# Kernel optimization log

Measured on AMD Instinct MI355X. Metric: run time of the kernel, lower is better.

The kernel has to match this reference:

```python
import jax, jax.numpy as jnp
import numpy as np

B, L, D, H = 2, 2048, 1024, 16
HD = D // H  # head dim = 64


def setup_inputs() -> dict:
    key = jax.random.key(0)
    ks = jax.random.split(key, 6)
    s = 0.02
    return {
        "hidden_states": jax.random.normal(ks[0], (B, L, D), jnp.float32),
        "attention_mask": jnp.zeros((B, 1, 1, L), jnp.float32),
        "Wq": jax.random.normal(ks[1], (D, D), jnp.float32) * s,
        "bq": jnp.zeros((D,), jnp.float32),
        "Wk": jax.random.normal(ks[2], (D, D), jnp.float32) * s,
        "bk": jnp.zeros((D,), jnp.float32),
        "Wv": jax.random.normal(ks[3], (D, D), jnp.float32) * s,
        "bv": jnp.zeros((D,), jnp.float32),
        "Wo": jax.random.normal(ks[4], (D, D), jnp.float32) * s,
        "bo": jnp.zeros((D,), jnp.float32),
    }


def reference(hidden_states, attention_mask, Wq, bq, Wk, bk, Wv, bv, Wo, bo):
    # Linear projections (torch Linear: x @ W.T + b; here W stored as [in,out])
    q = hidden_states @ Wq + bq  # [B,L,D]
    k = hidden_states @ Wk + bk
    v = hidden_states @ Wv + bv

    def split_heads(x):  # [B,L,D] -> [B,H,L,HD]
        return x.reshape(B, L, H, HD).transpose(0, 2, 1, 3)

    q, k, v = split_heads(q), split_heads(k), split_heads(v)

    scores = jnp.einsum("bhqd,bhkd->bhqk", q, k) / jnp.sqrt(
        jnp.asarray(HD, q.dtype)
    )
    scores = scores + attention_mask  # additive mask, broadcast [B,1,1,L]
    pdtype = scores.dtype
    # fp32 upcast around softmax, as in the original module
    probs = jax.nn.softmax(scores.astype(jnp.float32), axis=-1).astype(pdtype)
    # dropout prob = 0 (eval) -> identity; head_mask=None
    ctx = jnp.einsum("bhqk,bhkd->bhqd", probs, v)  # [B,H,L,HD]
    ctx = ctx.transpose(0, 2, 1, 3).reshape(B, L, D)
    out = ctx @ Wo + bo  # BertSelfOutput_preLN dense (dropout=0)
    return out
```

## Files before the change

### kernel.cpp

```cpp
#include <hip/hip_runtime.h>

#define BB 2
#define LL 2048
#define DDIM 1024
#define HH 16
#define HDIM 64
#define MM (BB*LL)
#define KK 1024
#define LOG2E 1.44269504f

typedef __attribute__((ext_vector_type(8))) short s8v;
typedef __attribute__((ext_vector_type(8))) unsigned short u8v;
typedef __attribute__((ext_vector_type(4))) float f4v;
typedef __attribute__((ext_vector_type(16))) float f16v;

__device__ __forceinline__ unsigned short f2bf(float f) {
    unsigned int u = __float_as_uint(f);
    u += 0x7fffu + ((u >> 16) & 1u);
    return (unsigned short)(u >> 16);
}

__device__ __forceinline__ float fexp2(float x) { return __builtin_amdgcn_exp2f(x); }

__device__ __forceinline__ void gld_lds16(const unsigned short* g, unsigned short* l) {
    __builtin_amdgcn_global_load_lds(
        (const __attribute__((address_space(1))) unsigned int*)g,
        (__attribute__((address_space(3))) unsigned int*)l, 16, 0, 0);
}

__global__ __launch_bounds__(256) void prep(
        const float* __restrict__ X,
        const float* __restrict__ Wq, const float* __restrict__ Wk,
        const float* __restrict__ Wv, const float* __restrict__ Wo,
        unsigned short* __restrict__ Xb,
        unsigned short* __restrict__ WqT, unsigned short* __restrict__ WkT,
        unsigned short* __restrict__ WvT, unsigned short* __restrict__ WoT) {
    __shared__ float lds[64][65];
    const int blk = blockIdx.x, t = threadIdx.x;
    if (blk < 4096) {
        int i = blk * 256 + t;
        float4 v = ((const float4*)X)[i];
        ushort4 r;
        r.x = f2bf(v.x); r.y = f2bf(v.y); r.z = f2bf(v.z); r.w = f2bf(v.w);
        ((ushort4*)Xb)[i] = r;
        return;
    }
    const int tb = blk - 4096;
    const int w = tb >> 8;
    const int tile = tb & 255;
    const int k0 = (tile >> 4) * 64, n0 = (tile & 15) * 64;
    const float* src; unsigned short* dst;
    switch (w) {
        case 0: src = Wq; dst = WqT; break;
        case 1: src = Wk; dst = WkT; break;
        case 2: src = Wv; dst = WvT; break;
        default: src = Wo; dst = WoT; break;
    }
    #pragma unroll
    for (int j = 0; j < 4; ++j) {
        int r = (t >> 4) + 16*j, c = (t & 15) * 4;
        float4 v = *(const float4*)(src + (size_t)(k0 + r) * DDIM + n0 + c);
        lds[r][c] = v.x; lds[r][c+1] = v.y; lds[r][c+2] = v.z; lds[r][c+3] = v.w;
    }
    __syncthreads();
    #pragma unroll
    for (int j = 0; j < 2; ++j) {
        int rr = (t >> 3) + 32*j, cc = (t & 7) * 8;
        u8v o;
        #pragma unroll
        for (int i = 0; i < 8; ++i) o[i] = f2bf(lds[cc + i][rr]);
        *(u8v*)(dst + (size_t)(n0 + rr) * KK + k0 + cc) = o;
    }
}

__device__ __forceinline__ void gemm_core(const unsigned short* __restrict__ A,
                                          const unsigned short* __restrict__ BT,
                                          int Mbase, int Nbase,
                                          unsigned short* As, unsigned short* Bs,
                                          f4v acc[4][4]) {
    const int t = threadIdx.x;
    const int lane = t & 63, wave = t >> 6;
    const int wm = wave & 1, wn = wave >> 1;
    const int l15 = lane & 15, quad = lane >> 4;
    const int srow = t >> 2, schunk = (t & 3) * 8;

    #pragma unroll
    for (int mt = 0; mt < 4; ++mt)
        #pragma unroll
        for (int nt = 0; nt < 4; ++nt)
            acc[mt][nt] = f4v{0.f, 0.f, 0.f, 0.f};

    const unsigned short* gA0 = A  + (size_t)(Mbase + srow)      * KK + schunk;
    const unsigned short* gA1 = A  + (size_t)(Mbase + 64 + srow) * KK + schunk;
    const unsigned short* gB0 = BT + (size_t)(Nbase + srow)      * KK + schunk;
    const unsigned short* gB1 = BT + (size_t)(Nbase + 64 + srow) * KK + schunk;

    for (int kb = 0; kb < KK; kb += 64) {
        __syncthreads();
        gld_lds16(gA0 + kb,      As + t*8);
        gld_lds16(gA1 + kb,      As + 2048 + t*8);
        gld_lds16(gA0 + kb + 32, As + 4096 + t*8);
        gld_lds16(gA1 + kb + 32, As + 4096 + 2048 + t*8);
        gld_lds16(gB0 + kb,      Bs + t*8);
        gld_lds16(gB1 + kb,      Bs + 2048 + t*8);
        gld_lds16(gB0 + kb + 32, Bs + 4096 + t*8);
        gld_lds16(gB1 + kb + 32, Bs + 4096 + 2048 + t*8);
        __syncthreads();
        #pragma unroll
        for (int kk = 0; kk < 2; ++kk) {
            const unsigned short* Ab = As + kk*4096;
            const unsigned short* Bb = Bs + kk*4096;
            s8v af[4], bfv[4];
            #pragma unroll
            for (int mt = 0; mt < 4; ++mt)
                af[mt] = *(const s8v*)(Ab + (wm*64 + mt*16 + l15)*32 + quad*8);
            #pragma unroll
            for (int nt = 0; nt < 4; ++nt)
                bfv[nt] = *(const s8v*)(Bb + (wn*64 + nt*16 + l15)*32 + quad*8);
            #pragma unroll
            for (int mt = 0; mt < 4; ++mt)
                #pragma unroll
                for (int nt = 0; nt < 4; ++nt)
                    acc[mt][nt] = __builtin_amdgcn_mfma_f32_16x16x32_bf16(af[mt], bfv[nt], acc[mt][nt], 0, 0, 0);
        }
    }
}

__global__ __launch_bounds__(256) void qkv_gemm(
        const unsigned short* __restrict__ Xb,
        const unsigned short* __restrict__ WqT, const unsigned short* __restrict__ WkT,
        const unsigned short* __restrict__ WvT,
        const float* __restrict__ bq, const float* __restrict__ bk, const float* __restrict__ bv,
        unsigned short* __restrict__ Qh, unsigned short* __restrict__ Kh,
        unsigned short* __restrict__ Vt) {
    __shared__ alignas(16) unsigned short As[128*64];
    __shared__ alignas(16) unsigned short Bs[128*64];
    const int mode = blockIdx.z;
    const unsigned short* BT = (mode == 0) ? WqT : (mode == 1) ? WkT : WvT;
    const float* bias        = (mode == 0) ? bq  : (mode == 1) ? bk  : bv;
    unsigned short* out      = (mode == 0) ? Qh  : (mode == 1) ? Kh  : Vt;
    const int Mbase = blockIdx.y * 128, Nbase = blockIdx.x * 128;

    f4v acc[4][4];
    gemm_core(Xb, BT, Mbase, Nbase, As, Bs, acc);

    const int lane = threadIdx.x & 63, wave = threadIdx.x >> 6;
    const int wm = wave & 1, wn = wave >> 1, l15 = lane & 15, quad = lane >> 4;
    #pragma unroll
    for (int mt = 0; mt < 4; ++mt)
        #pragma unroll
        for (int nt = 0; nt < 4; ++nt)
            #pragma unroll
            for (int r = 0; r < 4; ++r) {
                int gm = Mbase + wm*64 + mt*16 + quad*4 + r;
                int gn = Nbase + wn*64 + nt*16 + l15;
                float v = acc[mt][nt][r] + bias[gn];
                int bb = gm >> 11, ll = gm & 2047;
                int hh = gn >> 6,  dd = gn & 63;
                if (mode == 2)
                    out[((size_t)(bb*HH + hh)*HDIM + dd)*LL + ll] = f2bf(v);
                else
                    out[((size_t)(bb*HH + hh)*LL + ll)*HDIM + dd] = f2bf(v);
            }
}

__global__ __launch_bounds__(256) void attn(
        const unsigned short* __restrict__ Qh, const unsigned short* __restrict__ Kh,
        const unsigned short* __restrict__ Vt, const float* __restrict__ mask,
        unsigned short* __restrict__ ctx) {
    __shared__ alignas(16) unsigned short Ks[64*72];
    __shared__ alignas(16) unsigned short Vs[64*72];
    __shared__ alignas(16) unsigned short P [4*32*72];

    const int t = threadIdx.x, lane = t & 63, wave = t >> 6;
    const int l31 = lane & 31, hgrp = lane >> 5;

    const int n = blockIdx.x;
    const int bh = (n & 7) * 4 + ((n >> 3) & 3);
    const int qblk = n >> 5;
    const int b = bh >> 4, hh = bh & 15;

    const unsigned short* Qb = Qh + (size_t)bh * LL * HDIM;
    const unsigned short* Kb = Kh + (size_t)bh * LL * HDIM;
    const unsigned short* Vb = Vt + (size_t)bh * HDIM * LL;
    const float* mb = mask + (size_t)b * LL;
    const int q0 = qblk * 128 + wave * 32;
    unsigned short* Pw = P + wave * 32 * 72;

    const int srow = t >> 2, scol = (t & 3) * 16;

    s8v qf[4];
    #pragma unroll
    for (int hf = 0; hf < 4; ++hf)
        qf[hf] = *(const s8v*)(Qb + (size_t)(q0 + l31)*HDIM + hf*16 + hgrp*8);

    f16v o[2];
    #pragma unroll
    for (int nc = 0; nc < 2; ++nc)
        #pragma unroll
        for (int r = 0; r < 16; ++r) o[nc][r] = 0.f;
    float rs[16];
    #pragma unroll
    for (int r = 0; r < 16; ++r) rs[r] = 0.f;

    const float C1 = 0.125f * LOG2E;

    for (int kt = 0; kt < LL; kt += 64) {
        float4 ka  = *(const float4*)(Kb + (size_t)(kt + srow)*HDIM + scol);
        float4 kb2 = *(const float4*)(Kb + (size_t)(kt + srow)*HDIM + scol + 8);
        float4 va  = *(const float4*)(Vb + (size_t)srow*LL + kt + scol);
        float4 vb2 = *(const float4*)(Vb + (size_t)srow*LL + kt + scol + 8);
        float mv0 = mb[kt + l31] * LOG2E;
        float mv1 = mb[kt + 32 + l31] * LOG2E;

        __syncthreads();
        *(float4*)(Ks + srow*72 + scol)     = ka;
        *(float4*)(Ks + srow*72 + scol + 8) = kb2;
        *(float4*)(Vs + srow*72 + scol)     = va;
        *(float4*)(Vs + srow*72 + scol + 8) = vb2;
        __syncthreads();

        f16v sac[2];
        #pragma unroll
        for (int kc = 0; kc < 2; ++kc) {
            #pragma unroll
            for (int r = 0; r < 16; ++r) sac[kc][r] = 0.f;
            #pragma unroll
            for (int hf = 0; hf < 4; ++hf) {
                s8v kf = *(const s8v*)(Ks + (kc*32 + l31)*72 + hf*16 + hgrp*8);
                sac[kc] = __builtin_amdgcn_mfma_f32_32x32x16_bf16(qf[hf], kf, sac[kc], 0, 0, 0);
            }
        }
        #pragma unroll
        for (int kc = 0; kc < 2; ++kc) {
            float mvv = kc ? mv1 : mv0;
            #pragma unroll
            for (int r = 0; r < 16; ++r) {
                float p = fexp2(sac[kc][r] * C1 + mvv);
                rs[r] += p;
                int row = (r & 3) + 8*(r >> 2) + 4*hgrp;
                Pw[row*72 + kc*32 + l31] = f2bf(p);
            }
        }
        #pragma unroll
        for (int kt16 = 0; kt16 < 4; ++kt16) {
            s8v pf = *(const s8v*)(Pw + l31*72 + kt16*16 + hgrp*8);
            #pragma unroll
            for (int nc = 0; nc < 2; ++nc) {
                s8v vf = *(const s8v*)(Vs + (nc*32 + l31)*72 + kt16*16 + hgrp*8);
                o[nc] = __builtin_amdgcn_mfma_f32_32x32x16_bf16(pf, vf, o[nc], 0, 0, 0);
            }
        }
    }

    #pragma unroll
    for (int r = 0; r < 16; ++r) {
        float s0 = rs[r];
        s0 += __shfl_xor(s0, 1);
        s0 += __shfl_xor(s0, 2);
        s0 += __shfl_xor(s0, 4);
        s0 += __shfl_xor(s0, 8);
        s0 += __shfl_xor(s0, 16);
        rs[r] = 1.0f / s0;
    }
    #pragma unroll
    for (int r = 0; r < 16; ++r) {
        int row = (r & 3) + 8*(r >> 2) + 4*hgrp;
        int q = q0 + row;
        size_t base = ((size_t)b*LL + q)*DDIM + hh*HDIM;
        #pragma unroll
        for (int nc = 0; nc < 2; ++nc)
            ctx[base + nc*32 + l31] = f2bf(o[nc][r] * rs[r]);
    }
}

__global__ __launch_bounds__(256) void out_gemm(
        const unsigned short* __restrict__ Cb, const unsigned short* __restrict__ WoT,
        const float* __restrict__ bo, float* __restrict__ out) {
    __shared__ alignas(16) unsigned short As[128*64];
    __shared__ alignas(16) unsigned short Bs[64*64];
    const int t = threadIdx.x;
    const int lane = t & 63, wave = t >> 6;
    const int wm = wave & 1, wn = wave >> 1;
    const int l15 = lane & 15, quad = lane >> 4;
    const int srow = t >> 2, schunk = (t & 3) * 8;
    const int Mbase = blockIdx.y * 128, Nbase = blockIdx.x * 64;

    f4v acc[4][2];
    #pragma unroll
    for (int mt = 0; mt < 4; ++mt)
        #pragma unroll
        for (int nt = 0; nt < 2; ++nt)
            acc[mt][nt] = f4v{0.f, 0.f, 0.f, 0.f};

    const unsigned short* gA0 = Cb  + (size_t)(Mbase + srow)      * KK + schunk;
    const unsigned short* gA1 = Cb  + (size_t)(Mbase + 64 + srow) * KK + schunk;
    const unsigned short* gB0 = WoT + (size_t)(Nbase + srow)      * KK + schunk;

    for (int kb = 0; kb < KK; kb += 64) {
        __syncthreads();
        gld_lds16(gA0 + kb,      As + t*8);
        gld_lds16(gA1 + kb,      As + 2048 + t*8);
        gld_lds16(gA0 + kb + 32, As + 4096 + t*8);
        gld_lds16(gA1 + kb + 32, As + 4096 + 2048 + t*8);
        gld_lds16(gB0 + kb,      Bs + t*8);
        gld_lds16(gB0 + kb + 32, Bs + 2048 + t*8);
        __syncthreads();
        #pragma unroll
        for (int kk = 0; kk < 2; ++kk) {
            const unsigned short* Ab = As + kk*4096;
            const unsigned short* Bb = Bs + kk*2048;
            s8v af[4], bfv[2];
            #pragma unroll
            for (int mt = 0; mt < 4; ++mt)
                af[mt] = *(const s8v*)(Ab + (wm*64 + mt*16 + l15)*32 + quad*8);
            #pragma unroll
            for (int nt = 0; nt < 2; ++nt)
                bfv[nt] = *(const s8v*)(Bb + (wn*32 + nt*16 + l15)*32 + quad*8);
            #pragma unroll
            for (int mt = 0; mt < 4; ++mt)
                #pragma unroll
                for (int nt = 0; nt < 2; ++nt)
                    acc[mt][nt] = __builtin_amdgcn_mfma_f32_16x16x32_bf16(af[mt], bfv[nt], acc[mt][nt], 0, 0, 0);
        }
    }

    #pragma unroll
    for (int mt = 0; mt < 4; ++mt)
        #pragma unroll
        for (int nt = 0; nt < 2; ++nt)
            #pragma unroll
            for (int r = 0; r < 4; ++r) {
                int gm = Mbase + wm*64 + mt*16 + quad*4 + r;
                int gn = Nbase + wn*32 + nt*16 + l15;
                out[(size_t)gm*DDIM + gn] = acc[mt][nt][r] + bo[gn];
            }
}

extern "C" void kernel_launch(void* const* d_in, const int* in_sizes, int n_in,
                              void* d_out, int out_size, void* d_ws, size_t ws_size,
                              hipStream_t stream) {
    const float* X    = (const float*)d_in[0];
    const float* mask = (const float*)d_in[1];
    const float* Wq   = (const float*)d_in[2];
    const float* bq   = (const float*)d_in[3];
    const float* Wk   = (const float*)d_in[4];
    const float* bk   = (const float*)d_in[5];
    const float* Wv   = (const float*)d_in[6];
    const float* bv   = (const float*)d_in[7];
    const float* Wo   = (const float*)d_in[8];
    const float* bo   = (const float*)d_in[9];
    float* out = (float*)d_out;

    char* ws = (char*)d_ws;
    unsigned short* Xb  = (unsigned short*)(ws);
    unsigned short* WqT = (unsigned short*)(ws + (8u  << 20));
    unsigned short* WkT = (unsigned short*)(ws + (10u << 20));
    unsigned short* WvT = (unsigned short*)(ws + (12u << 20));
    unsigned short* WoT = (unsigned short*)(ws + (14u << 20));
    unsigned short* Qh  = (unsigned short*)(ws + (16u << 20));
    unsigned short* Kh  = (unsigned short*)(ws + (24u << 20));
    unsigned short* Vt  = (unsigned short*)(ws + (32u << 20));
    unsigned short* Cb  = Xb;

    prep     <<<dim3(5120),    dim3(256), 0, stream>>>(X, Wq, Wk, Wv, Wo, Xb, WqT, WkT, WvT, WoT);
    qkv_gemm <<<dim3(8,32,3),  dim3(256), 0, stream>>>(Xb, WqT, WkT, WvT, bq, bk, bv, Qh, Kh, Vt);
    attn     <<<dim3(512),     dim3(256), 0, stream>>>(Qh, Kh, Vt, mask, Cb);
    out_gemm <<<dim3(16,32),   dim3(256), 0, stream>>>(Cb, WoT, bo, out);
}
```

Baseline: 226.0 us.

## Stage QKV epilogue through LDS for vector stores, halve GEMM K-step

The QKV GEMM epilogue now writes biased bf16 results into shared memory in two halves, then emits 16-byte vectorized global stores. For V this performs the head transpose in LDS instead of scattered 2-byte strided writes. Both GEMMs drop from a 64-wide to a 32-wide K step with smaller LDS tiles, which lowers LDS use and may raise occupancy but doubles the number of barriers. The attention P conversion to bf16 now truncates instead of rounding, which saves a few ALU ops at a small accuracy cost.

New measurement: 222.9 us. About the same (-1.4%).

```diff
diff --git a/kernel.cpp b/kernel.cpp
--- a/kernel.cpp
+++ b/kernel.cpp
@@ -94,35 +94,30 @@
     const unsigned short* gA1 = A  + (size_t)(Mbase + 64 + srow) * KK + schunk;
     const unsigned short* gB0 = BT + (size_t)(Nbase + srow)      * KK + schunk;
     const unsigned short* gB1 = BT + (size_t)(Nbase + 64 + srow) * KK + schunk;
-
-    for (int kb = 0; kb < KK; kb += 64) {
-        __syncthreads();
-        gld_lds16(gA0 + kb,      As + t*8);
-        gld_lds16(gA1 + kb,      As + 2048 + t*8);
-        gld_lds16(gA0 + kb + 32, As + 4096 + t*8);
-        gld_lds16(gA1 + kb + 32, As + 4096 + 2048 + t*8);
-        gld_lds16(gB0 + kb,      Bs + t*8);
-        gld_lds16(gB1 + kb,      Bs + 2048 + t*8);
-        gld_lds16(gB0 + kb + 32, Bs + 4096 + t*8);
-        gld_lds16(gB1 + kb + 32, Bs + 4096 + 2048 + t*8);
-        __syncthreads();
-        #pragma unroll
-        for (int kk = 0; kk < 2; ++kk) {
-            const unsigned short* Ab = As + kk*4096;
-            const unsigned short* Bb = Bs + kk*4096;
-            s8v af[4], bfv[4];
-            #pragma unroll
-            for (int mt = 0; mt < 4; ++mt)
-                af[mt] = *(const s8v*)(Ab + (wm*64 + mt*16 + l15)*32 + quad*8);
+    unsigned short* lA0 = As + t*8;
+    unsigned short* lA1 = As + 64*32 + t*8;
+    unsigned short* lB0 = Bs + t*8;
+    unsigned short* lB1 = Bs + 64*32 + t*8;
+
+    for (int kb = 0; kb < KK; kb += 32) {
+        __syncthreads();
+        gld_lds16(gA0 + kb, lA0);
+        gld_lds16(gA1 + kb, lA1);
+        gld_lds16(gB0 + kb, lB0);
+        gld_lds16(gB1 + kb, lB1);
+        __syncthreads();
+        s8v af[4], bfv[4];
+        #pragma unroll
+        for (int mt = 0; mt < 4; ++mt)
+            af[mt] = *(const s8v*)(As + (wm*64 + mt*16 + l15)*32 + quad*8);
+        #pragma unroll
+        for (int nt = 0; nt < 4; ++nt)
+            bfv[nt] = *(const s8v*)(Bs + (wn*64 + nt*16 + l15)*32 + quad*8);
+        #pragma unroll
+        for (int mt = 0; mt < 4; ++mt)
             #pragma unroll
             for (int nt = 0; nt < 4; ++nt)
-                bfv[nt] = *(const s8v*)(Bb + (wn*64 + nt*16 + l15)*32 + quad*8);
-            #pragma unroll
-            for (int mt = 0; mt < 4; ++mt)
-                #pragma unroll
-                for (int nt = 0; nt < 4; ++nt)
-                    acc[mt][nt] = __builtin_amdgcn_mfma_f32_16x16x32_bf16(af[mt], bfv[nt], acc[mt][nt], 0, 0, 0);
-        }
+                acc[mt][nt] = __builtin_amdgcn_mfma_f32_16x16x32_bf16(af[mt], bfv[nt], acc[mt][nt], 0, 0, 0);
     }
 }
 
@@ -133,8 +128,9 @@
         const float* __restrict__ bq, const float* __restrict__ bk, const float* __restrict__ bv,
         unsigned short* __restrict__ Qh, unsigned short* __restrict__ Kh,
         unsigned short* __restrict__ Vt) {
-    __shared__ alignas(16) unsigned short As[128*64];
-    __shared__ alignas(16) unsigned short Bs[128*64];
+    __shared__ alignas(16) unsigned short smem[64*136 > 128*64 ? 64*136 : 128*64];
+    unsigned short* As = smem;
+    unsigned short* Bs = smem + 128*32;
     const int mode = blockIdx.z;
     const unsigned short* BT = (mode == 0) ? WqT : (mode == 1) ? WkT : WvT;
     const float* bias        = (mode == 0) ? bq  : (mode == 1) ? bk  : bv;
@@ -144,24 +140,59 @@
     f4v acc[4][4];
     gemm_core(Xb, BT, Mbase, Nbase, As, Bs, acc);
 
-    const int lane = threadIdx.x & 63, wave = threadIdx.x >> 6;
+    const int t = threadIdx.x;
+    const int lane = t & 63, wave = t >> 6;
     const int wm = wave & 1, wn = wave >> 1, l15 = lane & 15, quad = lane >> 4;
-    #pragma unroll
-    for (int mt = 0; mt < 4; ++mt)
-        #pragma unroll
-        for (int nt = 0; nt < 4; ++nt)
-            #pragma unroll
-            for (int r = 0; r < 4; ++r) {
-                int gm = Mbase + wm*64 + mt*16 + quad*4 + r;
-                int gn = Nbase + wn*64 + nt*16 + l15;
-                float v = acc[mt][nt][r] + bias[gn];
-                int bb = gm >> 11, ll = gm & 2047;
-                int hh = gn >> 6,  dd = gn & 63;
-                if (mode == 2)
-                    out[((size_t)(bb*HH + hh)*HDIM + dd)*LL + ll] = f2bf(v);
-                else
-                    out[((size_t)(bb*HH + hh)*LL + ll)*HDIM + dd] = f2bf(v);
-            }
+
+    float bl[4];
+    #pragma unroll
+    for (int nt = 0; nt < 4; ++nt) bl[nt] = bias[Nbase + wn*64 + nt*16 + l15];
+
+    #pragma unroll
+    for (int h2 = 0; h2 < 2; ++h2) {
+        __syncthreads();
+        if (wm == h2) {
+            #pragma unroll
+            for (int mt = 0; mt < 4; ++mt)
+                #pragma unroll
+                for (int nt = 0; nt < 4; ++nt)
+                    #pragma unroll
+                    for (int r = 0; r < 4; ++r) {
+                        int trow = mt*16 + quad*4 + r;
+                        int fcol = wn*64 + nt*16 + l15;
+                        smem[trow*136 + fcol] = f2bf(acc[mt][nt][r] + bl[nt]);
+                    }
+        }
+        __syncthreads();
+        const int gmbase = Mbase + h2*64;
+        if (mode == 2) {
+            int f = t >> 1, tc = (t & 1) * 32;
+            int gn = Nbase + f;
+            int hh = gn >> 6, dd = gn & 63;
+            int gm0 = gmbase + tc;
+            int bb = gm0 >> 11, ll0 = gm0 & 2047;
+            unsigned short* dst = out + ((size_t)(bb*HH + hh)*HDIM + dd)*LL + ll0;
+            #pragma unroll
+            for (int c = 0; c < 4; ++c) {
+                u8v o8;
+                #pragma unroll
+                for (int i = 0; i < 8; ++i)
+                    o8[i] = smem[(tc + c*8 + i)*136 + f];
+                *(u8v*)(dst + c*8) = o8;
+            }
+        } else {
+            int tt = t >> 2, fc = (t & 3) * 32;
+            int gm = gmbase + tt;
+            int bb = gm >> 11, ll = gm & 2047;
+            #pragma unroll
+            for (int c = 0; c < 4; ++c) {
+                int gn = Nbase + fc + c*8;
+                int hh = gn >> 6, dd = gn & 63;
+                u8v o8 = *(u8v*)(smem + tt*136 + fc + c*8);
+                *(u8v*)(out + ((size_t)(bb*HH + hh)*LL + ll)*HDIM + dd) = o8;
+            }
+        }
+    }
 }
 
 __global__ __launch_bounds__(256) void attn(
@@ -239,7 +270,7 @@
                 float p = fexp2(sac[kc][r] * C1 + mvv);
                 rs[r] += p;
                 int row = (r & 3) + 8*(r >> 2) + 4*hgrp;
-                Pw[row*72 + kc*32 + l31] = f2bf(p);
+                Pw[row*72 + kc*32 + l31] = (unsigned short)(__float_as_uint(p) >> 16);
             }
         }
         #pragma unroll
@@ -277,8 +308,8 @@
 __global__ __launch_bounds__(256) void out_gemm(
         const unsigned short* __restrict__ Cb, const unsigned short* __restrict__ WoT,
         const float* __restrict__ bo, float* __restrict__ out) {
-    __shared__ alignas(16) unsigned short As[128*64];
-    __shared__ alignas(16) unsigned short Bs[64*64];
+    __shared__ alignas(16) unsigned short As[128*32];
+    __shared__ alignas(16) unsigned short Bs[64*32];
     const int t = threadIdx.x;
     const int lane = t & 63, wave = t >> 6;
     const int wm = wave & 1, wn = wave >> 1;
@@ -296,33 +327,28 @@
     const unsigned short* gA0 = Cb  + (size_t)(Mbase + srow)      * KK + schunk;
     const unsigned short* gA1 = Cb  + (size_t)(Mbase + 64 + srow) * KK + schunk;
     const unsigned short* gB0 = WoT + (size_t)(Nbase + srow)      * KK + schunk;
-
-    for (int kb = 0; kb < KK; kb += 64) {
-        __syncthreads();
-        gld_lds16(gA0 + kb,      As + t*8);
-        gld_lds16(gA1 + kb,      As + 2048 + t*8);
-        gld_lds16(gA0 + kb + 32, As + 4096 + t*8);
-        gld_lds16(gA1 + kb + 32, As + 4096 + 2048 + t*8);
-        gld_lds16(gB0 + kb,      Bs + t*8);
-        gld_lds16(gB0 + kb + 32, Bs + 2048 + t*8);
-        __syncthreads();
-        #pragma unroll
-        for (int kk = 0; kk < 2; ++kk) {
-            const unsigned short* Ab = As + kk*4096;
-            const unsigned short* Bb = Bs + kk*2048;
-            s8v af[4], bfv[2];
-            #pragma unroll
-            for (int mt = 0; mt < 4; ++mt)
-                af[mt] = *(const s8v*)(Ab + (wm*64 + mt*16 + l15)*32 + quad*8);
+    unsigned short* lA0 = As + t*8;
+    unsigned short* lA1 = As + 64*32 + t*8;
+    unsigned short* lB0 = Bs + t*8;
+
+    for (int kb = 0; kb < KK; kb += 32) {
+        __syncthreads();
+        gld_lds16(gA0 + kb, lA0);
+        gld_lds16(gA1 + kb, lA1);
+        gld_lds16(gB0 + kb, lB0);
+        __syncthreads();
+        s8v af[4], bfv[2];
+        #pragma unroll
+        for (int mt = 0; mt < 4; ++mt)
+            af[mt] = *(const s8v*)(As + (wm*64 + mt*16 + l15)*32 + quad*8);
+        #pragma unroll
+        for (int nt = 0; nt < 2; ++nt)
+            bfv[nt] = *(const s8v*)(Bs + (wn*32 + nt*16 + l15)*32 + quad*8);
+        #pragma unroll
+        for (int mt = 0; mt < 4; ++mt)
             #pragma unroll
             for (int nt = 0; nt < 2; ++nt)
-                bfv[nt] = *(const s8v*)(Bb + (wn*32 + nt*16 + l15)*32 + quad*8);
-            #pragma unroll
-            for (int mt = 0; mt < 4; ++mt)
-                #pragma unroll
-                for (int nt = 0; nt < 2; ++nt)
-                    acc[mt][nt] = __builtin_amdgcn_mfma_f32_16x16x32_bf16(af[mt], bfv[nt], acc[mt][nt], 0, 0, 0);
-        }
+                acc[mt][nt] = __builtin_amdgcn_mfma_f32_16x16x32_bf16(af[mt], bfv[nt], acc[mt][nt], 0, 0, 0);
     }
 
     #pragma unroll
```
